# Optimization experiments

Measured on AMD Instinct MI355X. Metric: run time of the kernel, lower is better.

The kernel has to match this reference:

```python
import jax, jax.numpy as jnp
import numpy as np
from jax import lax

N_IN, N_H = 3, 2
N_REC = N_IN + N_H  # 5 qubits in the recurrent cell


def _ry(theta):
    # theta: (B,) -> (B, 2, 2) complex64 RY matrices
    c = jnp.cos(theta * 0.5).astype(jnp.complex64)
    s = jnp.sin(theta * 0.5).astype(jnp.complex64)
    return jnp.stack([jnp.stack([c, -s], -1), jnp.stack([s, c], -1)], -2)


def _rot(phi, theta, omega):
    # PennyLane Rot(phi, theta, omega) = RZ(omega) @ RY(theta) @ RZ(phi)
    c = jnp.cos(theta * 0.5)
    s = jnp.sin(theta * 0.5)
    ep = jnp.exp(-0.5j * (phi + omega))  # e^{-i(phi+omega)/2}
    em = jnp.exp(0.5j * (phi - omega))   # e^{+i(phi-omega)/2}
    m = jnp.stack([jnp.stack([ep * c, -em * s], -1),
                   jnp.stack([jnp.conj(em) * s, jnp.conj(ep) * c], -1)], -2)
    return m.astype(jnp.complex64)


def _apply1q(state, U, wire, n):
    # state: (B, 2**n); wire 0 is most significant (PennyLane convention)
    L, R = 2 ** wire, 2 ** (n - wire - 1)
    st = state.reshape(-1, L, 2, R)
    sub = 'bij,bljr->blir' if U.ndim == 3 else 'ij,bljr->blir'
    return jnp.einsum(sub, U, st).reshape(state.shape)


def _cnot_perm(c, t, n):
    # CNOT is a fixed basis permutation: flip target bit where control bit set
    cbit, tbit = 1 << (n - 1 - c), 1 << (n - 1 - t)
    idx = np.arange(2 ** n)
    return np.where(idx & cbit, idx ^ tbit, idx)


def _entangle(state, weights, n):
    # StronglyEntanglingLayers: per-wire Rot, then CNOT ring with range r
    n_layers = weights.shape[0]
    for l in range(n_layers):
        for w in range(n):
            state = _apply1q(state, _rot(weights[l, w, 0], weights[l, w, 1], weights[l, w, 2]), w, n)
        r = (l % (n - 1)) + 1
        for w in range(n):
            state = state[:, _cnot_perm(w, (w + r) % n, n)]
    return state


def _expz(state, wire, n):
    # <Z_wire> = P(0) - P(1)
    L, R = 2 ** wire, 2 ** (n - wire - 1)
    p = (state.real ** 2 + state.imag ** 2).reshape(-1, L, 2, R).sum((1, 3))
    return p[:, 0] - p[:, 1]


def _init_state(batch, n):
    s = jnp.zeros((batch, 2 ** n), jnp.complex64)
    return s.at[:, 0].set(1.0)


def _cell(x, h, w_rec):
    # batched qrnn_cell: RY-encode x on wires 0..2, h on wires 3..4, entangle, read Z(3),Z(4)
    state = _init_state(x.shape[0], N_REC)
    for i in range(N_IN):
        state = _apply1q(state, _ry(x[:, i]), i, N_REC)
    for j in range(N_H):
        state = _apply1q(state, _ry(h[:, j]), N_IN + j, N_REC)
    state = _entangle(state, w_rec, N_REC)
    return jnp.stack([_expz(state, N_IN + j, N_REC) for j in range(N_H)], -1)


def _readout(h, w_out):
    # batched qnn_readout: 2-qubit circuit, Z(0) expval
    state = _init_state(h.shape[0], N_H)
    for j in range(N_H):
        state = _apply1q(state, _ry(h[:, j]), j, N_H)
    state = _entangle(state, w_out, N_H)
    return _expz(state, 0, N_H)[:, None]


def setup_inputs() -> dict:
    key = jax.random.key(0)
    k1, k2, k3 = jax.random.split(key, 3)
    T, B = 32, 8192
    x_seq = jax.random.normal(k1, (T, B, N_IN), jnp.float32)
    w_rec = jax.random.normal(k2, (2, N_REC, 3), jnp.float32)
    w_out = jax.random.normal(k3, (2, N_H, 3), jnp.float32)
    return {"x_seq": x_seq, "w_rec": w_rec, "w_out": w_out}


def reference(x_seq, w_rec, w_out):
    B = x_seq.shape[1]

    def step(h, xt):
        return _cell(xt, h, w_rec), None

    h, _ = lax.scan(step, jnp.zeros((B, N_H), jnp.float32), x_seq)
    return _readout(h, w_out)  # (B, 1)
```

## Files before the change

### kernel.cpp

```cpp
#include <hip/hip_runtime.h>
#include <math.h>


constexpr int cnot_ct(int idx, int c, int t) {
    return (idx & (1 << (4 - c))) ? (idx ^ (1 << (4 - t))) : idx;
}
constexpr int Pfwd_ct(int x, int r) {
    for (int w = 4; w >= 0; --w) x = cnot_ct(x, w, (w + r) % 5);
    return x;
}
constexpr int Pinv_ct(int x, int r) {
    for (int w = 0; w <= 4; ++w) x = cnot_ct(x, w, (w + r) % 5);
    return x;
}
static_assert(Pinv_ct(Pfwd_ct(13, 1), 1) == 13, "inv1");
static_assert(Pinv_ct(Pfwd_ct(22, 2), 2) == 22, "inv2");

constexpr int GMASK[10] = {16, 8, 4, 2, 1,
                           Pfwd_ct(16,1), Pfwd_ct(8,1), Pfwd_ct(4,1), Pfwd_ct(2,1), Pfwd_ct(1,1)};
constexpr int fmask_l1(int pb) {
    int f = 0;
    for (int b = 0; b < 5; ++b) if ((Pinv_ct(1 << b, 1) >> pb) & 1) f |= 1 << b;
    return f;
}
constexpr int FMASK[10] = {16, 8, 4, 2, 1,
                           fmask_l1(4), fmask_l1(3), fmask_l1(2), fmask_l1(1), fmask_l1(0)};
constexpr int cinv_ct(int x) { return Pinv_ct(Pinv_ct(x, 1), 2); }
constexpr int fmask_fin(int pb) {
    int f = 0;
    for (int b = 0; b < 5; ++b) if ((cinv_ct(1 << b) >> pb) & 1) f |= 1 << b;
    return f;
}
constexpr int SF3 = fmask_fin(1);
constexpr int SF4 = fmask_fin(0);

constexpr bool gates_straddle() {
    for (int g = 0; g < 10; ++g)
        if (!(__builtin_popcount(GMASK[g] & FMASK[g]) & 1)) return false;
    return true;
}
static_assert(gates_straddle(), "GMASK/FMASK straddle");

constexpr unsigned span3_ct(int a, int b, int c) {
    unsigned m = 0;
    for (int i = 0; i < 8; ++i) {
        int v = ((i & 1) ? a : 0) ^ ((i & 2) ? b : 0) ^ ((i & 4) ? c : 0);
        m |= 1u << v;
    }
    return m;
}
static_assert(span3_ct(1, 2, 7) == 0xFFu, "butterfly {1,2,7} spans lanes 0..7");

__device__ __forceinline__ int pinv_rt(int x, int r) {
    #pragma unroll
    for (int w = 0; w < 5; ++w) {
        int cbit = 1 << (4 - w), tbit = 1 << (4 - ((w + r) % 5));
        if (x & cbit) x ^= tbit;
    }
    return x;
}

template<int CTRL> __device__ __forceinline__ float dppf(float x) {
    return __int_as_float(__builtin_amdgcn_mov_dpp(__float_as_int(x), CTRL, 0xF, 0xF, true));
}
template<int PL> __device__ __forceinline__ float mvf(float x) {
    if constexpr (PL == 1)      return dppf<0xB1>(x);
    else if constexpr (PL == 2) return dppf<0x4E>(x);
    else if constexpr (PL == 7) return dppf<0x141>(x);
    else if constexpr (PL == 8) return dppf<0x128>(x);
    else { static_assert(PL == 1 || PL == 2 || PL == 7 || PL == 8, "mask"); return x; }
}

template<int g>
__device__ __forceinline__ void gate_full(float (&ar)[32], float (&ai)[32],
                                          float c, float s) {
    constexpr int m = GMASK[g], F = FMASK[g];
    #pragma unroll
    for (int i = 0; i < 32; ++i) {
        if ((__builtin_popcount(i & F) & 1) == 0) {
            const int j = i ^ m;
            const float r0 = ar[i], i0 = ai[i], r1 = ar[j], i1 = ai[j];
            ar[i] = c * r0 - s * r1;  ai[i] = c * i0 - s * i1;
            ar[j] = s * r0 + c * r1;  ai[j] = s * i0 + c * i1;
        }
    }
}

__global__ __launch_bounds__(256, 3) void qrnn_fused(
    const float* __restrict__ x_seq, const float* __restrict__ w_rec,
    const float* __restrict__ w_out, float* __restrict__ out, int B) {

    __shared__ __align__(16) float4 xs4[16 * 33];
    __shared__ __align__(16) float A2s[18 * 28];
    __shared__ float CgS[10], SgS[10];
    __shared__ float P0c[32], P0s[32], E1c[32], E1s[32];
    __shared__ float RC[16];
    __shared__ __align__(16) float Cm_pool[16 * 19 * 33];
    float* const Qs  = Cm_pool;
    float* const P1s = Cm_pool + 512;

    const int tloc = threadIdx.x;
    const int grp  = tloc >> 4;
    const int k    = tloc & 15;
    const int b0   = blockIdx.x * 16;
    const int b    = b0 + grp;

    #pragma unroll
    for (int qq = 0; qq < 2; ++qq) {
        const int p = tloc + qq * 256;
        const int ts = p >> 4, lbs = p & 15;
        const int gidx = (ts * B + (b0 + lbs)) * 3;
        float4 v;
        v.x = x_seq[gidx]; v.y = x_seq[gidx + 1]; v.z = x_seq[gidx + 2]; v.w = 0.f;
        xs4[lbs * 33 + ts] = v;
    }

    if (tloc < 10) {
        const float th = w_rec[(tloc / 5) * 15 + (tloc % 5) * 3 + 1];
        CgS[tloc] = cosf(0.5f * th);
        SgS[tloc] = sinf(0.5f * th);
    } else if (tloc >= 32 && tloc < 96) {
        const int idx = tloc - 32;
        const int i = idx & 31;
        float ang = 0.f;
        if (idx < 32) {
            #pragma unroll
            for (int w = 0; w < 5; ++w)
                ang += (((i >> (4 - w)) & 1) ? 0.5f : -0.5f) * w_rec[w * 3 + 0];
            P0c[i] = cosf(ang); P0s[i] = sinf(ang);
        } else {
            const int j = pinv_rt(i, 1);
            #pragma unroll
            for (int w = 0; w < 5; ++w) {
                ang += (((i >> (4 - w)) & 1) ? 0.5f : -0.5f) * w_rec[w * 3 + 2];
                ang += (((j >> (4 - w)) & 1) ? 0.5f : -0.5f) * w_rec[15 + w * 3 + 0];
            }
            E1c[i] = cosf(ang); E1s[i] = sinf(ang);
        }
    } else if (tloc >= 96 && tloc < 100) {
        const int g = tloc - 96;
        const int li = g >> 1, w = g & 1;
        const float phi = w_out[li * 6 + w * 3 + 0];
        const float the = w_out[li * 6 + w * 3 + 1];
        const float ome = w_out[li * 6 + w * 3 + 2];
        const float cs = cosf(0.5f * the), ss = sinf(0.5f * the);
        const float cp = cosf(0.5f * (phi + ome)), sp = sinf(0.5f * (phi + ome));
        const float cm = cosf(0.5f * (phi - ome)), sm = sinf(0.5f * (phi - ome));
        RC[g * 4 + 0] = cp * cs;
        RC[g * 4 + 1] = -sp * cs;
        RC[g * 4 + 2] = cm * ss;
        RC[g * 4 + 3] = sm * ss;
    }
    __syncthreads();

    if (tloc < 243) {
        const int d0 = tloc / 81, d1 = (tloc / 27) % 3, d2 = (tloc / 9) % 3,
                  d3 = (tloc / 3) % 3, d4 = tloc % 3;
        const float C3[3] = {1.f, 0.5f, 0.5f};
        const float S3[3] = {0.f, 0.86602540378443865f, -0.86602540378443865f};
        const float f0c = C3[d0], f0s = S3[d0], f1c = C3[d1], f1s = S3[d1],
                    f2c = C3[d2], f2s = S3[d2], f3c = C3[d3], f3s = S3[d3],
                    f4c = C3[d4], f4s = S3[d4];

        float ar[32], ai[32];
        #pragma unroll
        for (int i = 0; i < 32; ++i) {
            const float bb = ((i & 16) ? f0s : f0c) * ((i & 8) ? f1s : f1c) *
                             ((i & 4) ? f2s : f2c) * ((i & 2) ? f3s : f3c) *
                             ((i & 1) ? f4s : f4c);
            ar[i] = bb * P0c[i]; ai[i] = bb * P0s[i];
        }
        gate_full<0>(ar, ai, CgS[0], SgS[0]);
        gate_full<1>(ar, ai, CgS[1], SgS[1]);
        gate_full<2>(ar, ai, CgS[2], SgS[2]);
        gate_full<3>(ar, ai, CgS[3], SgS[3]);
        gate_full<4>(ar, ai, CgS[4], SgS[4]);
        #pragma unroll
        for (int i = 0; i < 32; ++i) {
            const float nr = ar[i] * E1c[i] - ai[i] * E1s[i];
            const float ni = ar[i] * E1s[i] + ai[i] * E1c[i];
            ar[i] = nr; ai[i] = ni;
        }
        gate_full<5>(ar, ai, CgS[5], SgS[5]);
        gate_full<6>(ar, ai, CgS[6], SgS[6]);
        gate_full<7>(ar, ai, CgS[7], SgS[7]);
        gate_full<8>(ar, ai, CgS[8], SgS[8]);
        gate_full<9>(ar, ai, CgS[9], SgS[9]);
        float q0 = 0.f, q1 = 0.f;
        #pragma unroll
        for (int i = 0; i < 32; ++i) {
            const float p = ar[i] * ar[i] + ai[i] * ai[i];
            q0 += (__builtin_popcount(i & SF3) & 1) ? -p : p;
            q1 += (__builtin_popcount(i & SF4) & 1) ? -p : p;
        }
        Qs[tloc * 2 + 0] = q0; Qs[tloc * 2 + 1] = q1;
    }
    __syncthreads();

    const float W[3][3] = {{1.f/3.f, 1.f/3.f, 1.f/3.f},
                           {2.f/3.f, -1.f/3.f, -1.f/3.f},
                           {0.f, 0.57735026918962576f, -0.57735026918962576f}};
    for (int o = tloc; o < 486; o += 256) {
        const int j = o & 1, e = o >> 1;
        const int d012 = e / 9, pq = e % 9, p = pq / 3, q = pq % 3;
        float acc = 0.f;
        #pragma unroll
        for (int d3 = 0; d3 < 3; ++d3) {
            const float wp = W[p][d3];
            #pragma unroll
            for (int d4 = 0; d4 < 3; ++d4)
                acc = fmaf(wp * W[q][d4], Qs[(d012 * 9 + d3 * 3 + d4) * 2 + j], acc);
        }
        P1s[(d012 * 9 + pq) * 2 + j] = acc;
    }
    __syncthreads();

    for (int o = tloc; o < 486; o += 256) {
        const int row = o / 27, col = o % 27;
        const int j = row / 9, pq = row % 9;
        const int a0 = col / 9, a1 = (col / 3) % 3, a2 = col % 3;
        float acc = 0.f;
        #pragma unroll
        for (int dd0 = 0; dd0 < 3; ++dd0) {
            const float w0 = W[a0][dd0];
            #pragma unroll
            for (int dd1 = 0; dd1 < 3; ++dd1) {
                const float w01 = w0 * W[a1][dd1];
                #pragma unroll
                for (int dd2 = 0; dd2 < 3; ++dd2)
                    acc = fmaf(w01 * W[a2][dd2],
                               P1s[((dd0 * 9 + dd1 * 3 + dd2) * 9 + pq) * 2 + j], acc);
            }
        }
        A2s[row * 28 + col] = acc;
    }
    if (tloc < 18) A2s[tloc * 28 + 27] = 0.f;
    __syncthreads();

    constexpr float Kf = 0.15915494309189535f;
    float Xb0[28], Xb1[28];
    #pragma unroll
    for (int tt = 0; tt < 2; ++tt) {
        float* Xb = tt ? Xb1 : Xb0;
        const float4 xv = xs4[grp * 33 + k + 16 * tt];
        const float cx0 = __builtin_amdgcn_cosf(xv.x * Kf);
        const float sx0 = __builtin_amdgcn_cosf(fmaf(xv.x, Kf, -0.25f));
        const float cx1 = __builtin_amdgcn_cosf(xv.y * Kf);
        const float sx1 = __builtin_amdgcn_cosf(fmaf(xv.y, Kf, -0.25f));
        const float cx2 = __builtin_amdgcn_cosf(xv.z * Kf);
        const float sx2 = __builtin_amdgcn_cosf(fmaf(xv.z, Kf, -0.25f));
        Xb[0] = 1.f;  Xb[1] = cx2;       Xb[2] = sx2;
        Xb[3] = cx1;  Xb[4] = cx1 * cx2; Xb[5] = cx1 * sx2;
        Xb[6] = sx1;  Xb[7] = sx1 * cx2; Xb[8] = sx1 * sx2;
        #pragma unroll
        for (int i = 0; i < 9; ++i) { Xb[9 + i] = cx0 * Xb[i]; Xb[18 + i] = sx0 * Xb[i]; }
        Xb[27] = 0.f;
    }
    {
        const float4* Ap = (const float4*)A2s;
        float* const Cmg = Cm_pool + grp * (19 * 33);
        float4 av[7], nv[7];
        #pragma unroll
        for (int i = 0; i < 7; ++i) av[i] = Ap[i];
        #pragma unroll 1
        for (int r = 0; r < 18; ++r) {
            if (r < 17) {
                #pragma unroll
                for (int i = 0; i < 7; ++i) nv[i] = Ap[(r + 1) * 7 + i];
            }
            float a00 = 0.f, a01 = 0.f, a10 = 0.f, a11 = 0.f;
            #pragma unroll
            for (int i = 0; i < 7; ++i) {
                a00 = fmaf(av[i].x, Xb0[4*i+0], a00); a00 = fmaf(av[i].y, Xb0[4*i+1], a00);
                a01 = fmaf(av[i].z, Xb0[4*i+2], a01); a01 = fmaf(av[i].w, Xb0[4*i+3], a01);
                a10 = fmaf(av[i].x, Xb1[4*i+0], a10); a10 = fmaf(av[i].y, Xb1[4*i+1], a10);
                a11 = fmaf(av[i].z, Xb1[4*i+2], a11); a11 = fmaf(av[i].w, Xb1[4*i+3], a11);
            }
            Cmg[r * 33 + k]      = a00 + a01;
            Cmg[r * 33 + k + 16] = a10 + a11;
            #pragma unroll
            for (int i = 0; i < 7; ++i) av[i] = nv[i];
        }
        Cmg[18 * 33 + k] = 0.f; Cmg[18 * 33 + k + 16] = 0.f;
    }

    const int jj = k >> 3;
    const int term = (k & 7) + 1;
    const int rowA = jj * 9 + term;
    const int rowB = (k == 0) ? 0 : ((k == 8) ? 9 : 18);
    const int p = term / 3, q = term % 3;
    const float* CA_ptr = Cm_pool + grp * (19 * 33) + rowA * 33;
    const float* CB_ptr = Cm_pool + grp * (19 * 33) + rowB * 33;

    float h0 = 0.f, h1 = 0.f;
    float CA = CA_ptr[0], CB = CB_ptr[0];
    #pragma unroll 1
    for (int t = 0; t < 32; ++t) {
        const int tn = (t < 31) ? t + 1 : 31;
        const float CAn = CA_ptr[tn], CBn = CB_ptr[tn];
        const float ch0 = __builtin_amdgcn_cosf(h0 * Kf);
        const float sh0 = __builtin_amdgcn_cosf(fmaf(h0, Kf, -0.25f));
        const float ch1 = __builtin_amdgcn_cosf(h1 * Kf);
        const float sh1 = __builtin_amdgcn_cosf(fmaf(h1, Kf, -0.25f));
        const float u = (p == 1) ? ch0 : ((p == 2) ? sh0 : 1.f);
        const float v = (q == 1) ? ch1 : ((q == 2) ? sh1 : 1.f);
        float val = fmaf(CA, u * v, CB);
        val += mvf<1>(val);
        val += mvf<2>(val);
        val += mvf<7>(val);
        const float other = mvf<8>(val);
        h0 = (k & 8) ? other : val;
        h1 = (k & 8) ? val : other;
        CA = CAn; CB = CBn;
    }

    constexpr float K2 = 0.5f * 0.15915494309189535f;
    const float ch0 = __builtin_amdgcn_cosf(h0 * K2);
    const float sh0 = __builtin_amdgcn_cosf(fmaf(h0, K2, -0.25f));
    const float ch1 = __builtin_amdgcn_cosf(h1 * K2);
    const float sh1 = __builtin_amdgcn_cosf(fmaf(h1, K2, -0.25f));
    float vr0 = ch0 * ch1, vr1 = ch0 * sh1, vr2 = sh0 * ch1, vr3 = sh0 * sh1;
    float vi0 = 0.f, vi1 = 0.f, vi2 = 0.f, vi3 = 0.f;

    #pragma unroll
    for (int li = 0; li < 2; ++li) {
        #pragma unroll
        for (int w = 0; w < 2; ++w) {
            const int g = li * 2 + w;
            const float are = RC[g*4+0], aim = RC[g*4+1];
            const float bre = RC[g*4+2], bim = RC[g*4+3];
            #define AP2(r0, i0, r1, i1) do {                                  \
                float n0r = are*(r0) - aim*(i0) - bre*(r1) + bim*(i1);        \
                float n0i = are*(i0) + aim*(r0) - bre*(i1) - bim*(r1);        \
                float n1r = bre*(r0) + bim*(i0) + are*(r1) + aim*(i1);        \
                float n1i = bre*(i0) - bim*(r0) + are*(i1) - aim*(r1);        \
                r0 = n0r; i0 = n0i; r1 = n1r; i1 = n1i; } while (0)
            if (w == 0) { AP2(vr0, vi0, vr2, vi2); AP2(vr1, vi1, vr3, vi3); }
            else        { AP2(vr0, vi0, vr1, vi1); AP2(vr2, vi2, vr3, vi3); }
            #undef AP2
        }
        float tr1 = vr2, ti1 = vi2, tr2 = vr3, ti2 = vi3, tr3 = vr1, ti3 = vi1;
        vr1 = tr1; vi1 = ti1; vr2 = tr2; vi2 = ti2; vr3 = tr3; vi3 = ti3;
    }

    const float outv = (vr0 * vr0 + vi0 * vi0 + vr1 * vr1 + vi1 * vi1) -
                       (vr2 * vr2 + vi2 * vi2 + vr3 * vr3 + vi3 * vi3);
    if (k == 0) out[b] = outv;
}

extern "C" void kernel_launch(void* const* d_in, const int* in_sizes, int n_in,
                              void* d_out, int out_size, void* d_ws, size_t ws_size,
                              hipStream_t stream) {
    const float* x_seq = (const float*)d_in[0];
    const float* w_rec = (const float*)d_in[1];
    const float* w_out = (const float*)d_in[2];
    float* out = (float*)d_out;

    const int B = out_size;
    const int grid = (B * 16) / 256;

    hipLaunchKernelGGL(qrnn_fused, dim3(grid), dim3(256), 0, stream,
                       x_seq, w_rec, w_out, out, B);
}
```

Before: 76.76 us.

## Preload recurrence coefficients into registers and cut per-step transcendentals

The 32-step recurrence now preloads all per-step coefficients into registers and is fully unrolled. Each lane evaluates only the two cosines it needs, using a per-lane scale and phase offset instead of computing four and selecting. The row-by-row coefficient build switches to a two-buffer double-buffered load of A2 rows. Small constant tables are replaced by select expressions to avoid local-memory arrays, Q stores are vectorised, and launch bounds drop from 3 to 2 blocks per SM, trading occupancy for a larger register budget.

```diff
diff --git a/kernel.cpp b/kernel.cpp
--- a/kernel.cpp
+++ b/kernel.cpp
@@ -60,6 +60,14 @@
     return x;
 }
 
+__device__ __forceinline__ float Wsel(int r, int d) {
+    float b, c;
+    if (d == 0)      { b =  2.f / 3.f; c = 0.f; }
+    else if (d == 1) { b = -1.f / 3.f; c =  0.57735026918962576f; }
+    else             { b = -1.f / 3.f; c = -0.57735026918962576f; }
+    return (r == 0) ? (1.f / 3.f) : ((r == 1) ? b : c);
+}
+
 template<int CTRL> __device__ __forceinline__ float dppf(float x) {
     return __int_as_float(__builtin_amdgcn_mov_dpp(__float_as_int(x), CTRL, 0xF, 0xF, true));
 }
@@ -86,7 +94,7 @@
     }
 }
 
-__global__ __launch_bounds__(256, 3) void qrnn_fused(
+__global__ __launch_bounds__(256, 2) void qrnn_fused(
     const float* __restrict__ x_seq, const float* __restrict__ w_rec,
     const float* __restrict__ w_out, float* __restrict__ out, int B) {
 
@@ -156,11 +164,17 @@
     if (tloc < 243) {
         const int d0 = tloc / 81, d1 = (tloc / 27) % 3, d2 = (tloc / 9) % 3,
                   d3 = (tloc / 3) % 3, d4 = tloc % 3;
-        const float C3[3] = {1.f, 0.5f, 0.5f};
-        const float S3[3] = {0.f, 0.86602540378443865f, -0.86602540378443865f};
-        const float f0c = C3[d0], f0s = S3[d0], f1c = C3[d1], f1s = S3[d1],
-                    f2c = C3[d2], f2s = S3[d2], f3c = C3[d3], f3s = S3[d3],
-                    f4c = C3[d4], f4s = S3[d4];
+        constexpr float S3v = 0.86602540378443865f;
+        const float f0c = (d0 == 0) ? 1.f : 0.5f;
+        const float f0s = (d0 == 0) ? 0.f : ((d0 == 1) ? S3v : -S3v);
+        const float f1c = (d1 == 0) ? 1.f : 0.5f;
+        const float f1s = (d1 == 0) ? 0.f : ((d1 == 1) ? S3v : -S3v);
+        const float f2c = (d2 == 0) ? 1.f : 0.5f;
+        const float f2s = (d2 == 0) ? 0.f : ((d2 == 1) ? S3v : -S3v);
+        const float f3c = (d3 == 0) ? 1.f : 0.5f;
+        const float f3s = (d3 == 0) ? 0.f : ((d3 == 1) ? S3v : -S3v);
+        const float f4c = (d4 == 0) ? 1.f : 0.5f;
+        const float f4s = (d4 == 0) ? 0.f : ((d4 == 1) ? S3v : -S3v);
 
         float ar[32], ai[32];
         #pragma unroll
@@ -193,23 +207,20 @@
             q0 += (__builtin_popcount(i & SF3) & 1) ? -p : p;
             q1 += (__builtin_popcount(i & SF4) & 1) ? -p : p;
         }
-        Qs[tloc * 2 + 0] = q0; Qs[tloc * 2 + 1] = q1;
+        *reinterpret_cast<float2*>(&Qs[tloc * 2]) = make_float2(q0, q1);
     }
     __syncthreads();
 
-    const float W[3][3] = {{1.f/3.f, 1.f/3.f, 1.f/3.f},
-                           {2.f/3.f, -1.f/3.f, -1.f/3.f},
-                           {0.f, 0.57735026918962576f, -0.57735026918962576f}};
     for (int o = tloc; o < 486; o += 256) {
         const int j = o & 1, e = o >> 1;
-        const int d012 = e / 9, pq = e % 9, p = pq / 3, q = pq % 3;
+        const int d012 = e / 9, pq = e % 9, pp = pq / 3, qq2 = pq % 3;
         float acc = 0.f;
         #pragma unroll
         for (int d3 = 0; d3 < 3; ++d3) {
-            const float wp = W[p][d3];
+            const float wp = Wsel(pp, d3);
             #pragma unroll
             for (int d4 = 0; d4 < 3; ++d4)
-                acc = fmaf(wp * W[q][d4], Qs[(d012 * 9 + d3 * 3 + d4) * 2 + j], acc);
+                acc = fmaf(wp * Wsel(qq2, d4), Qs[(d012 * 9 + d3 * 3 + d4) * 2 + j], acc);
         }
         P1s[(d012 * 9 + pq) * 2 + j] = acc;
     }
@@ -222,13 +233,13 @@
         float acc = 0.f;
         #pragma unroll
         for (int dd0 = 0; dd0 < 3; ++dd0) {
-            const float w0 = W[a0][dd0];
+            const float w0 = Wsel(a0, dd0);
             #pragma unroll
             for (int dd1 = 0; dd1 < 3; ++dd1) {
-                const float w01 = w0 * W[a1][dd1];
+                const float w01 = w0 * Wsel(a1, dd1);
                 #pragma unroll
                 for (int dd2 = 0; dd2 < 3; ++dd2)
-                    acc = fmaf(w01 * W[a2][dd2],
+                    acc = fmaf(w01 * Wsel(a2, dd2),
                                P1s[((dd0 * 9 + dd1 * 3 + dd2) * 9 + pq) * 2 + j], acc);
             }
         }
@@ -259,27 +270,45 @@
     {
         const float4* Ap = (const float4*)A2s;
         float* const Cmg = Cm_pool + grp * (19 * 33);
-        float4 av[7], nv[7];
-        #pragma unroll
-        for (int i = 0; i < 7; ++i) av[i] = Ap[i];
+        float4 bA[7], bB[7];
+        #pragma unroll
+        for (int i = 0; i < 7; ++i) bA[i] = Ap[i];
+        #pragma unroll
+        for (int i = 0; i < 7; ++i) bB[i] = Ap[7 + i];
         #pragma unroll 1
-        for (int r = 0; r < 18; ++r) {
-            if (r < 17) {
+        for (int r = 0; r < 18; r += 2) {
+            {
+                float a00 = 0.f, a01 = 0.f, a10 = 0.f, a11 = 0.f;
                 #pragma unroll
-                for (int i = 0; i < 7; ++i) nv[i] = Ap[(r + 1) * 7 + i];
+                for (int i = 0; i < 7; ++i) {
+                    a00 = fmaf(bA[i].x, Xb0[4*i+0], a00); a00 = fmaf(bA[i].y, Xb0[4*i+1], a00);
+                    a01 = fmaf(bA[i].z, Xb0[4*i+2], a01); a01 = fmaf(bA[i].w, Xb0[4*i+3], a01);
+                    a10 = fmaf(bA[i].x, Xb1[4*i+0], a10); a10 = fmaf(bA[i].y, Xb1[4*i+1], a10);
+                    a11 = fmaf(bA[i].z, Xb1[4*i+2], a11); a11 = fmaf(bA[i].w, Xb1[4*i+3], a11);
+                }
+                Cmg[r * 33 + k]      = a00 + a01;
+                Cmg[r * 33 + k + 16] = a10 + a11;
+                if (r < 16) {
+                    #pragma unroll
+                    for (int i = 0; i < 7; ++i) bA[i] = Ap[(r + 2) * 7 + i];
+                }
             }
-            float a00 = 0.f, a01 = 0.f, a10 = 0.f, a11 = 0.f;
-            #pragma unroll
-            for (int i = 0; i < 7; ++i) {
-                a00 = fmaf(av[i].x, Xb0[4*i+0], a00); a00 = fmaf(av[i].y, Xb0[4*i+1], a00);
-                a01 = fmaf(av[i].z, Xb0[4*i+2], a01); a01 = fmaf(av[i].w, Xb0[4*i+3], a01);
-                a10 = fmaf(av[i].x, Xb1[4*i+0], a10); a10 = fmaf(av[i].y, Xb1[4*i+1], a10);
-                a11 = fmaf(av[i].z, Xb1[4*i+2], a11); a11 = fmaf(av[i].w, Xb1[4*i+3], a11);
+            {
+                float a00 = 0.f, a01 = 0.f, a10 = 0.f, a11 = 0.f;
+                #pragma unroll
+                for (int i = 0; i < 7; ++i) {
+                    a00 = fmaf(bB[i].x, Xb0[4*i+0], a00); a00 = fmaf(bB[i].y, Xb0[4*i+1], a00);
+                    a01 = fmaf(bB[i].z, Xb0[4*i+2], a01); a01 = fmaf(bB[i].w, Xb0[4*i+3], a01);
+                    a10 = fmaf(bB[i].x, Xb1[4*i+0], a10); a10 = fmaf(bB[i].y, Xb1[4*i+1], a10);
+                    a11 = fmaf(bB[i].z, Xb1[4*i+2], a11); a11 = fmaf(bB[i].w, Xb1[4*i+3], a11);
+                }
+                Cmg[(r + 1) * 33 + k]      = a00 + a01;
+                Cmg[(r + 1) * 33 + k + 16] = a10 + a11;
+                if (r < 16) {
+                    #pragma unroll
+                    for (int i = 0; i < 7; ++i) bB[i] = Ap[(r + 3) * 7 + i];
+                }
             }
-            Cmg[r * 33 + k]      = a00 + a01;
-            Cmg[r * 33 + k + 16] = a10 + a11;
-            #pragma unroll
-            for (int i = 0; i < 7; ++i) av[i] = nv[i];
         }
         Cmg[18 * 33 + k] = 0.f; Cmg[18 * 33 + k + 16] = 0.f;
     }
@@ -292,26 +321,27 @@
     const float* CA_ptr = Cm_pool + grp * (19 * 33) + rowA * 33;
     const float* CB_ptr = Cm_pool + grp * (19 * 33) + rowB * 33;
 
+    float CAr[32], CBr[32];
+    #pragma unroll
+    for (int t = 0; t < 32; ++t) { CAr[t] = CA_ptr[t]; CBr[t] = CB_ptr[t]; }
+
+    const float Kfu = (p == 0) ? 0.f : Kf;
+    const float bu  = (p == 2) ? -0.25f : 0.f;
+    const float Kfv = (q == 0) ? 0.f : Kf;
+    const float bv  = (q == 2) ? -0.25f : 0.f;
+
     float h0 = 0.f, h1 = 0.f;
-    float CA = CA_ptr[0], CB = CB_ptr[0];
-    #pragma unroll 1
+    #pragma unroll
     for (int t = 0; t < 32; ++t) {
-        const int tn = (t < 31) ? t + 1 : 31;
-        const float CAn = CA_ptr[tn], CBn = CB_ptr[tn];
-        const float ch0 = __builtin_amdgcn_cosf(h0 * Kf);
-        const float sh0 = __builtin_amdgcn_cosf(fmaf(h0, Kf, -0.25f));
-        const float ch1 = __builtin_amdgcn_cosf(h1 * Kf);
-        const float sh1 = __builtin_amdgcn_cosf(fmaf(h1, Kf, -0.25f));
-        const float u = (p == 1) ? ch0 : ((p == 2) ? sh0 : 1.f);
-        const float v = (q == 1) ? ch1 : ((q == 2) ? sh1 : 1.f);
-        float val = fmaf(CA, u * v, CB);
+        const float u = __builtin_amdgcn_cosf(fmaf(h0, Kfu, bu));
+        const float v = __builtin_amdgcn_cosf(fmaf(h1, Kfv, bv));
+        float val = fmaf(CAr[t], u * v, CBr[t]);
         val += mvf<1>(val);
         val += mvf<2>(val);
         val += mvf<7>(val);
         const float other = mvf<8>(val);
         h0 = (k & 8) ? other : val;
         h1 = (k & 8) ? val : other;
-        CA = CAn; CB = CBn;
     }
 
     constexpr float K2 = 0.5f * 0.15915494309189535f;
```

New measurement: 73.68 us. -4.0%, faster.
